# Performance work log

Hardware: AMD Instinct MI355X
Metric: run time of the kernel (lower is better)

Reference implementation:

```python
import jax, jax.numpy as jnp
import numpy as np

N = 100000
E = 1600000
D_IN = 128
D_OUT = 128
BN_EPS = 1e-5


def setup_inputs() -> dict:
    key = jax.random.key(0)
    k = jax.random.split(key, 8)
    feats = jax.random.normal(k[0], (N, D_IN), dtype=jnp.float32)
    src = jax.random.randint(k[1], (E,), 0, N, dtype=jnp.int32)
    dst = jax.random.randint(k[2], (E,), 0, N, dtype=jnp.int32)
    # GraphConv weight (in, out) + bias, residual Linear, batchnorm affine
    W = jax.random.normal(k[3], (D_IN, D_OUT), dtype=jnp.float32) / np.sqrt(D_IN)
    b = jnp.zeros((D_OUT,), dtype=jnp.float32)
    Wr = jax.random.normal(k[4], (D_IN, D_OUT), dtype=jnp.float32) / np.sqrt(D_IN)
    br = jnp.zeros((D_OUT,), dtype=jnp.float32)
    gamma = jnp.ones((D_OUT,), dtype=jnp.float32)
    beta = jnp.zeros((D_OUT,), dtype=jnp.float32)
    return {"feats": feats, "src": src, "dst": dst, "W": W, "b": b,
            "Wr": Wr, "br": br, "gamma": gamma, "beta": beta}


def reference(feats, src, dst, W, b, Wr, br, gamma, beta):
    ones = jnp.ones((src.shape[0],), dtype=feats.dtype)
    out_deg = jax.ops.segment_sum(ones, src, num_segments=N)
    in_deg = jax.ops.segment_sum(ones, dst, num_segments=N)
    norm_src = jax.lax.rsqrt(jnp.maximum(out_deg, 1.0))  # [N]
    norm_dst = jax.lax.rsqrt(jnp.maximum(in_deg, 1.0))   # [N]

    # GraphConv, norm='both' (in_feats == out_feats -> aggregate then matmul)
    h = feats * norm_src[:, None]
    agg = jax.ops.segment_sum(h[src], dst, num_segments=N)  # [N, D_IN]
    agg = agg * norm_dst[:, None]
    conv = jax.nn.relu(agg @ W + b)

    # residual linear + activation
    res = jax.nn.relu(feats @ Wr + br)
    y = conv + res  # dropout p=0 -> identity

    # BatchNorm1d (batch statistics, biased variance)
    mean = jnp.mean(y, axis=0)
    var = jnp.var(y, axis=0)
    y = (y - mean) * jax.lax.rsqrt(var + BN_EPS) * gamma + beta
    return y
```

## Files before the change

### kernel.cpp

```cpp
#include <hip/hip_runtime.h>

#define NN 100000
#define DD 128
#define EE 1600000
#define BN_EPS 1e-5f
#define NBLK 3125
#define NCH 2
#define CH 50000
#define CW (CH / 4)
#define NEB 64
#define EPB (EE / NEB)

using bf16x8 = __attribute__((ext_vector_type(8))) short;
using f32x4  = __attribute__((ext_vector_type(4))) float;

__device__ __forceinline__ unsigned short bf16r(float f) {
    unsigned u = __float_as_uint(f);
    u += 0x7FFF + ((u >> 16) & 1);
    return (unsigned short)(u >> 16);
}
__device__ __forceinline__ float bf2f(unsigned short h) {
    return __uint_as_float((unsigned)h << 16);
}

__global__ __launch_bounds__(1024) void hist_kernel(
    const int4* __restrict__ src4, const int4* __restrict__ dst4,
    unsigned char* __restrict__ outT8, unsigned char* __restrict__ inT8,
    unsigned char* __restrict__ lrank) {
    __shared__ unsigned outc[CW];
    __shared__ unsigned inc[CW];
    const int j = blockIdx.x & (NEB - 1);
    const int c = blockIdx.x >> 6;
    const int clo = c * CH;
    const int t = threadIdx.x;
    for (int i = t; i < CW; i += 1024) { outc[i] = 0; inc[i] = 0; }
    __syncthreads();
    const int base = j * (EPB / 4);
    for (int i = t; i < EPB / 4; i += 1024) {
        int4 s = src4[base + i];
        int4 d = dst4[base + i];
        int e = j * EPB + i * 4;
        unsigned sx = (unsigned)(s.x - clo);
        unsigned sy = (unsigned)(s.y - clo);
        unsigned sz = (unsigned)(s.z - clo);
        unsigned sw = (unsigned)(s.w - clo);
        if (sx < CH) atomicAdd(&outc[sx >> 2], 1u << ((sx & 3) * 8));
        if (sy < CH) atomicAdd(&outc[sy >> 2], 1u << ((sy & 3) * 8));
        if (sz < CH) atomicAdd(&outc[sz >> 2], 1u << ((sz & 3) * 8));
        if (sw < CH) atomicAdd(&outc[sw >> 2], 1u << ((sw & 3) * 8));
        unsigned dx = (unsigned)(d.x - clo);
        unsigned dy = (unsigned)(d.y - clo);
        unsigned dz = (unsigned)(d.z - clo);
        unsigned dw = (unsigned)(d.w - clo);
        if (dx < CH) { unsigned o = atomicAdd(&inc[dx >> 2], 1u << ((dx & 3) * 8)); lrank[e + 0] = (unsigned char)(o >> ((dx & 3) * 8)); }
        if (dy < CH) { unsigned o = atomicAdd(&inc[dy >> 2], 1u << ((dy & 3) * 8)); lrank[e + 1] = (unsigned char)(o >> ((dy & 3) * 8)); }
        if (dz < CH) { unsigned o = atomicAdd(&inc[dz >> 2], 1u << ((dz & 3) * 8)); lrank[e + 2] = (unsigned char)(o >> ((dz & 3) * 8)); }
        if (dw < CH) { unsigned o = atomicAdd(&inc[dw >> 2], 1u << ((dw & 3) * 8)); lrank[e + 3] = (unsigned char)(o >> ((dw & 3) * 8)); }
    }
    __syncthreads();
    unsigned* op = (unsigned*)(outT8 + (size_t)j * NN + clo);
    unsigned* ip = (unsigned*)(inT8 + (size_t)j * NN + clo);
    for (int i = t; i < CW; i += 1024) {
        op[i] = outc[i];
        ip[i] = inc[i];
    }
}

__global__ __launch_bounds__(1024) void scan1_kernel(
    const unsigned char* __restrict__ outT8, unsigned char* __restrict__ inT8,
    int* __restrict__ partial, int* __restrict__ blocksum,
    float* __restrict__ ns, float* __restrict__ nd) {
    __shared__ int s[1024];
    int t = threadIdx.x;
    int idx = blockIdx.x * 1024 + t;
    int run_in = 0;
    if (idx < NN) {
        int run_out = 0;
#pragma unroll 8
        for (int j = 0; j < NEB; ++j) {
            run_out += (int)outT8[(size_t)j * NN + idx];
            int ci = (int)inT8[(size_t)j * NN + idx];
            inT8[(size_t)j * NN + idx] = (unsigned char)run_in;
            run_in += ci;
        }
        ns[idx] = rsqrtf(fmaxf((float)run_out, 1.0f));
        nd[idx] = rsqrtf(fmaxf((float)run_in, 1.0f));
    }
    int v = run_in;
    s[t] = v;
    __syncthreads();
    for (int off = 1; off < 1024; off <<= 1) {
        int x = (t >= off) ? s[t - off] : 0;
        __syncthreads();
        s[t] += x;
        __syncthreads();
    }
    if (idx < NN) partial[idx] = s[t] - v;
    if (t == 1023) blocksum[blockIdx.x] = s[t];
}

__global__ void scan23_kernel(const int* __restrict__ partial, const int* __restrict__ blocksum,
                              int* __restrict__ row_ofs) {
    __shared__ int s[128];
    int t = threadIdx.x;
    if (t < 128) s[t] = (t < 98) ? blocksum[t] : 0;
    __syncthreads();
    for (int off = 1; off < 128; off <<= 1) {
        int x = (t < 128 && t >= off) ? s[t - off] : 0;
        __syncthreads();
        if (t < 128) s[t] += x;
        __syncthreads();
    }
    int i = blockIdx.x * blockDim.x + t;
    if (i < NN) {
        int bk = i >> 10;
        row_ofs[i] = partial[i] + s[bk] - blocksum[bk];
        if (i == 0) row_ofs[NN] = EE;
    }
}

__global__ void fill4_kernel(const int4* __restrict__ src4, const int4* __restrict__ dst4,
                             const unsigned char* __restrict__ baseT8,
                             const uchar4* __restrict__ lrank4,
                             const int* __restrict__ row_ofs, int* __restrict__ e_src) {
    int i = blockIdx.x * blockDim.x + threadIdx.x;
    if (i < EE / 4) {
        int4 s = src4[i];
        int4 d = dst4[i];
        uchar4 r = lrank4[i];
        int j = (i * 4) / EPB;
        const unsigned char* bT = baseT8 + (size_t)j * NN;
        e_src[row_ofs[d.x] + (int)bT[d.x] + (int)r.x] = s.x;
        e_src[row_ofs[d.y] + (int)bT[d.y] + (int)r.y] = s.y;
        e_src[row_ofs[d.z] + (int)bT[d.z] + (int)r.z] = s.z;
        e_src[row_ofs[d.w] + (int)bT[d.w] + (int)r.w] = s.w;
    }
}

__global__ void cvt_kernel(const float4* __restrict__ feats4, const float* __restrict__ ns,
                           ushort4* __restrict__ fb4) {
    int i = blockIdx.x * blockDim.x + threadIdx.x;
    if (i < NN * 32) {
        float s = ns[i >> 5];
        float4 v = feats4[i];
        ushort4 h;
        h.x = bf16r(v.x * s);
        h.y = bf16r(v.y * s);
        h.z = bf16r(v.z * s);
        h.w = bf16r(v.w * s);
        fb4[i] = h;
    }
}

__global__ void prepw_kernel(const float* __restrict__ W, const float* __restrict__ Wr,
                             unsigned short* __restrict__ wb) {
    int g = blockIdx.x >> 5;
    int f = blockIdx.x & 31;
    int ct = f >> 2, ks = f & 3;
    int l = threadIdx.x;
    const float* G = g ? Wr : W;
    unsigned short* hi = wb + (((size_t)(g * 2 + 0) * 32 + f) * 64 + l) * 8;
    unsigned short* lo = wb + (((size_t)(g * 2 + 1) * 32 + f) * 64 + l) * 8;
    for (int i = 0; i < 8; ++i) {
        int k = ks * 32 + (l >> 4) * 8 + i;
        int col = ct * 16 + (l & 15);
        float w = G[k * 128 + col];
        unsigned uh = __float_as_uint(w) & 0xFFFF0000u;
        hi[i] = (unsigned short)(uh >> 16);
        lo[i] = bf16r(w - __uint_as_float(uh));
    }
}

__device__ __forceinline__ void accum8(float* a, int4 u) {
    a[0] += __uint_as_float((unsigned)u.x << 16);
    a[1] += __uint_as_float((unsigned)u.x & 0xFFFF0000u);
    a[2] += __uint_as_float((unsigned)u.y << 16);
    a[3] += __uint_as_float((unsigned)u.y & 0xFFFF0000u);
    a[4] += __uint_as_float((unsigned)u.z << 16);
    a[5] += __uint_as_float((unsigned)u.z & 0xFFFF0000u);
    a[6] += __uint_as_float((unsigned)u.w << 16);
    a[7] += __uint_as_float((unsigned)u.w & 0xFFFF0000u);
}

__global__ __launch_bounds__(256, 6) void gather_kernel(
    const int4* __restrict__ fbi, const float* __restrict__ nd,
    const int* __restrict__ row_ofs, const int* __restrict__ e_src,
    float* __restrict__ y) {
    const int lane = threadIdx.x & 15;
    const int grp = threadIdx.x >> 4;
    const int node = blockIdx.x * 16 + grp;
    const int beg = row_ofs[node];
    const int end = row_ofs[node + 1];

    float a0[8] = {0.f, 0.f, 0.f, 0.f, 0.f, 0.f, 0.f, 0.f};
    float a1[8] = {0.f, 0.f, 0.f, 0.f, 0.f, 0.f, 0.f, 0.f};

    for (int e = beg; e < end; e += 16) {
        int cnt = end - e;
        if (cnt > 16) cnt = 16;
        int myidx = (lane < cnt) ? e_src[e + lane] : 0;
        int j = 0;
        for (; j + 7 < cnt; j += 8) {
            int s0 = __shfl(myidx, j, 16);
            int s1 = __shfl(myidx, j + 1, 16);
            int s2 = __shfl(myidx, j + 2, 16);
            int s3 = __shfl(myidx, j + 3, 16);
            int s4 = __shfl(myidx, j + 4, 16);
            int s5 = __shfl(myidx, j + 5, 16);
            int s6 = __shfl(myidx, j + 6, 16);
            int s7 = __shfl(myidx, j + 7, 16);
            int4 u0 = fbi[(size_t)s0 * 16 + lane];
            int4 u1 = fbi[(size_t)s1 * 16 + lane];
            int4 u2 = fbi[(size_t)s2 * 16 + lane];
            int4 u3 = fbi[(size_t)s3 * 16 + lane];
            int4 u4 = fbi[(size_t)s4 * 16 + lane];
            int4 u5 = fbi[(size_t)s5 * 16 + lane];
            int4 u6 = fbi[(size_t)s6 * 16 + lane];
            int4 u7 = fbi[(size_t)s7 * 16 + lane];
            accum8(a0, u0);
            accum8(a1, u1);
            accum8(a0, u2);
            accum8(a1, u3);
            accum8(a0, u4);
            accum8(a1, u5);
            accum8(a0, u6);
            accum8(a1, u7);
        }
        for (; j + 3 < cnt; j += 4) {
            int s0 = __shfl(myidx, j, 16);
            int s1 = __shfl(myidx, j + 1, 16);
            int s2 = __shfl(myidx, j + 2, 16);
            int s3 = __shfl(myidx, j + 3, 16);
            int4 u0 = fbi[(size_t)s0 * 16 + lane];
            int4 u1 = fbi[(size_t)s1 * 16 + lane];
            int4 u2 = fbi[(size_t)s2 * 16 + lane];
            int4 u3 = fbi[(size_t)s3 * 16 + lane];
            accum8(a0, u0);
            accum8(a1, u1);
            accum8(a0, u2);
            accum8(a1, u3);
        }
        for (; j < cnt; ++j) {
            int s0 = __shfl(myidx, j, 16);
            int4 u0 = fbi[(size_t)s0 * 16 + lane];
            accum8(a0, u0);
        }
    }

    float snd = nd[node];
    float4 o0, o1;
    o0.x = (a0[0] + a1[0]) * snd;
    o0.y = (a0[1] + a1[1]) * snd;
    o0.z = (a0[2] + a1[2]) * snd;
    o0.w = (a0[3] + a1[3]) * snd;
    o1.x = (a0[4] + a1[4]) * snd;
    o1.y = (a0[5] + a1[5]) * snd;
    o1.z = (a0[6] + a1[6]) * snd;
    o1.w = (a0[7] + a1[7]) * snd;
    ((float4*)y)[(size_t)node * 32 + lane * 2] = o0;
    ((float4*)y)[(size_t)node * 32 + lane * 2 + 1] = o1;
}

__device__ __forceinline__ void hilo4(float4 v, ushort4& h, ushort4& l) {
    unsigned u0 = __float_as_uint(v.x) & 0xFFFF0000u;
    unsigned u1 = __float_as_uint(v.y) & 0xFFFF0000u;
    unsigned u2 = __float_as_uint(v.z) & 0xFFFF0000u;
    unsigned u3 = __float_as_uint(v.w) & 0xFFFF0000u;
    h.x = (unsigned short)(u0 >> 16);
    h.y = (unsigned short)(u1 >> 16);
    h.z = (unsigned short)(u2 >> 16);
    h.w = (unsigned short)(u3 >> 16);
    l.x = bf16r(v.x - __uint_as_float(u0));
    l.y = bf16r(v.y - __uint_as_float(u1));
    l.z = bf16r(v.z - __uint_as_float(u2));
    l.w = bf16r(v.w - __uint_as_float(u3));
}

__global__ __launch_bounds__(256, 4) void gemm_kernel(
    const float4* __restrict__ feats4,
    const unsigned short* __restrict__ wb,
    const float* __restrict__ b, const float* __restrict__ br,
    float* y, float* __restrict__ part_sum, float* __restrict__ part_sq) {
    __shared__ unsigned short AsH[32 * 128];
    __shared__ unsigned short AsL[32 * 128];
    __shared__ unsigned short FsH[32 * 128];
    __shared__ unsigned short FsL[32 * 128];

    const int tid = threadIdx.x;
    const int block_row = blockIdx.x * 32;
    const float4* agg4 = (const float4*)y;

    for (int i = tid; i < 1024; i += 256) {
        int r = i >> 5;
        int c4 = i & 31;
        size_t g = (size_t)(block_row + r) * 32 + c4;
        float4 a = agg4[g];
        float4 f = feats4[g];
        int off = (r * 256 + ((c4 * 8) ^ ((r & 7) << 4))) >> 1;
        ushort4 h, l;
        hilo4(a, h, l);
        *(ushort4*)(&AsH[off]) = h;
        *(ushort4*)(&AsL[off]) = l;
        hilo4(f, h, l);
        *(ushort4*)(&FsH[off]) = h;
        *(ushort4*)(&FsL[off]) = l;
    }
    __syncthreads();

    const int w = tid >> 6;
    const int l = tid & 63;
    const int lr = l & 15;
    const int lh = l >> 4;
    const int ct0 = w * 2;
    const bf16x8* WB = (const bf16x8*)wb;

    const f32x4 fzero = {0.f, 0.f, 0.f, 0.f};
    f32x4 aC[2][2], aR[2][2];
#pragma unroll
    for (int r = 0; r < 2; ++r)
#pragma unroll
        for (int c = 0; c < 2; ++c) { aC[r][c] = fzero; aR[r][c] = fzero; }

#pragma unroll 1
    for (int ks = 0; ks < 4; ++ks) {
        bf16x8 ah[2], al[2], fh[2], fl[2];
#pragma unroll
        for (int r = 0; r < 2; ++r) {
            int row = r * 16 + lr;
            int off = (row * 256 + ((ks * 64 + lh * 16) ^ ((row & 7) << 4))) >> 1;
            ah[r] = *(const bf16x8*)(&AsH[off]);
            al[r] = *(const bf16x8*)(&AsL[off]);
            fh[r] = *(const bf16x8*)(&FsH[off]);
            fl[r] = *(const bf16x8*)(&FsL[off]);
        }
#pragma unroll
        for (int c = 0; c < 2; ++c) {
            int fr = (ct0 + c) * 4 + ks;
            bf16x8 wh  = WB[(0 * 32 + fr) * 64 + l];
            bf16x8 wl  = WB[(1 * 32 + fr) * 64 + l];
            bf16x8 wrh = WB[(2 * 32 + fr) * 64 + l];
            bf16x8 wrl = WB[(3 * 32 + fr) * 64 + l];
#pragma unroll
            for (int r = 0; r < 2; ++r) {
                aC[r][c] = __builtin_amdgcn_mfma_f32_16x16x32_bf16(ah[r], wh, aC[r][c], 0, 0, 0);
                aC[r][c] = __builtin_amdgcn_mfma_f32_16x16x32_bf16(al[r], wh, aC[r][c], 0, 0, 0);
                aC[r][c] = __builtin_amdgcn_mfma_f32_16x16x32_bf16(ah[r], wl, aC[r][c], 0, 0, 0);
                aR[r][c] = __builtin_amdgcn_mfma_f32_16x16x32_bf16(fh[r], wrh, aR[r][c], 0, 0, 0);
                aR[r][c] = __builtin_amdgcn_mfma_f32_16x16x32_bf16(fl[r], wrh, aR[r][c], 0, 0, 0);
                aR[r][c] = __builtin_amdgcn_mfma_f32_16x16x32_bf16(fh[r], wrl, aR[r][c], 0, 0, 0);
            }
        }
    }

#pragma unroll
    for (int c = 0; c < 2; ++c) {
        int col = (ct0 + c) * 16 + lr;
        float bv = b[col], brv = br[col];
        float cs = 0.f, cq = 0.f;
#pragma unroll
        for (int r = 0; r < 2; ++r) {
#pragma unroll
            for (int i = 0; i < 4; ++i) {
                float o = fmaxf(aC[r][c][i] + bv, 0.f) + fmaxf(aR[r][c][i] + brv, 0.f);
                int grow = block_row + r * 16 + lh * 4 + i;
                y[(size_t)grow * 128 + col] = o;
                cs += o;
                cq += o * o;
            }
        }
        cs += __shfl_xor(cs, 16); cs += __shfl_xor(cs, 32);
        cq += __shfl_xor(cq, 16); cq += __shfl_xor(cq, 32);
        if (lh == 0) {
            part_sum[(size_t)blockIdx.x * 128 + col] = cs;
            part_sq[(size_t)blockIdx.x * 128 + col] = cq;
        }
    }
}

__global__ __launch_bounds__(256) void colreduce_kernel(
    const float* __restrict__ part_sum, const float* __restrict__ part_sq,
    float* __restrict__ colsum, float* __restrict__ colsumsq) {
    int j = blockIdx.x;
    int t = threadIdx.x;
    float s = 0.f, q = 0.f;
    for (int bb = t; bb < NBLK; bb += 256) {
        s += part_sum[(size_t)bb * 128 + j];
        q += part_sq[(size_t)bb * 128 + j];
    }
#pragma unroll
    for (int off = 1; off < 64; off <<= 1) {
        s += __shfl_xor(s, off);
        q += __shfl_xor(q, off);
    }
    __shared__ float ss[4], qq[4];
    if ((t & 63) == 0) { ss[t >> 6] = s; qq[t >> 6] = q; }
    __syncthreads();
    if (t == 0) {
        colsum[j] = ss[0] + ss[1] + ss[2] + ss[3];
        colsumsq[j] = qq[0] + qq[1] + qq[2] + qq[3];
    }
}

__global__ void apply2_kernel(float4* __restrict__ y4,
                              const float* __restrict__ colsum, const float* __restrict__ colsumsq,
                              const float* __restrict__ gamma, const float* __restrict__ beta) {
    __shared__ float sc4[128], sh4[128];
    int t = threadIdx.x;
    if (t < 128) {
        const float inv_n = 1.0f / (float)NN;
        float mean = colsum[t] * inv_n;
        float var = colsumsq[t] * inv_n - mean * mean;
        float s = gamma[t] * rsqrtf(var + BN_EPS);
        sc4[t] = s;
        sh4[t] = beta[t] - mean * s;
    }
    __syncthreads();
    int i = blockIdx.x * 256 + t;
    if (i < NN * 32) {
        int c = (i & 31) * 4;
        float4 v = y4[i];
        v.x = v.x * sc4[c + 0] + sh4[c + 0];
        v.y = v.y * sc4[c + 1] + sh4[c + 1];
        v.z = v.z * sc4[c + 2] + sh4[c + 2];
        v.w = v.w * sc4[c + 3] + sh4[c + 3];
        y4[i] = v;
    }
}

extern "C" void kernel_launch(void* const* d_in, const int* in_sizes, int n_in,
                              void* d_out, int out_size, void* d_ws, size_t ws_size,
                              hipStream_t stream) {
    const float* feats = (const float*)d_in[0];
    const int* src = (const int*)d_in[1];
    const int* dst = (const int*)d_in[2];
    const float* W = (const float*)d_in[3];
    const float* b = (const float*)d_in[4];
    const float* Wr = (const float*)d_in[5];
    const float* br = (const float*)d_in[6];
    const float* gamma = (const float*)d_in[7];
    const float* beta = (const float*)d_in[8];
    float* y = (float*)d_out;

    char* ws = (char*)d_ws;
    unsigned char* outT8 = (unsigned char*)ws;
    unsigned char* inT8 = outT8 + (size_t)NEB * NN;
    unsigned char* lrank = inT8 + (size_t)NEB * NN;
    ushort4* fb4 = (ushort4*)ws;
    float* part_sum = (float*)lrank;
    float* part_sq = part_sum + (size_t)NBLK * 128;
    char* wsB = ws + (size_t)NN * 32 * 8;
    float* ns = (float*)wsB;
    float* nd = ns + NN;
    int* row_ofs = (int*)(nd + NN);
    int* partial = row_ofs + NN + 1;
    int* blocksum = partial + NN;
    int* e_src = blocksum + 128;
    float* colsum = (float*)(e_src + EE);
    float* colsumsq = colsum + DD;
    unsigned long long wbofs = (unsigned long long)((char*)(colsumsq + DD) - ws);
    wbofs = (wbofs + 255ull) & ~255ull;
    unsigned short* wb = (unsigned short*)(ws + wbofs);

    prepw_kernel<<<64, 64, 0, stream>>>(W, Wr, wb);
    hist_kernel<<<NCH * NEB, 1024, 0, stream>>>((const int4*)src, (const int4*)dst,
                                                outT8, inT8, lrank);
    scan1_kernel<<<98, 1024, 0, stream>>>(outT8, inT8, partial, blocksum, ns, nd);
    scan23_kernel<<<(NN + 255) / 256, 256, 0, stream>>>(partial, blocksum, row_ofs);
    fill4_kernel<<<(EE / 4 + 255) / 256, 256, 0, stream>>>((const int4*)src, (const int4*)dst,
                                                           inT8, (const uchar4*)lrank,
                                                           row_ofs, e_src);
    cvt_kernel<<<(NN * 32 + 255) / 256, 256, 0, stream>>>((const float4*)feats, ns, fb4);
    gather_kernel<<<NN / 16, 256, 0, stream>>>((const int4*)fb4, nd, row_ofs, e_src, y);
    gemm_kernel<<<NBLK, 256, 0, stream>>>((const float4*)feats, wb, b, br,
                                          y, part_sum, part_sq);
    colreduce_kernel<<<128, 256, 0, stream>>>(part_sum, part_sq, colsum, colsumsq);
    apply2_kernel<<<(NN * 32 + 255) / 256, 256, 0, stream>>>((float4*)y, colsum, colsumsq,
                                                             gamma, beta);
}
```

Measured before the change: 308.6 us.

## Fuse weight prep into hist kernel, chunk fill with LDS offsets, trim gather unroll

Weight splitting into bf16 hi/lo now runs as an extra block of the histogram kernel, which removes one launch. The edge fill kernel is restructured so each block handles one edge segment and a 25000-node destination chunk, with row offsets and base counts staged in shared memory. This replaces the scattered global lookups with LDS reads, but every block now rereads its edge segment four times. The 8-way unrolled loop in the gather kernel is removed, leaving the 4-way loop, which cuts register pressure at the cost of fewer loads in flight.

```diff
diff --git a/kernel.cpp b/kernel.cpp
--- a/kernel.cpp
+++ b/kernel.cpp
@@ -10,6 +10,7 @@
 #define CW (CH / 4)
 #define NEB 64
 #define EPB (EE / NEB)
+#define FCH 25000
 
 using bf16x8 = __attribute__((ext_vector_type(8))) short;
 using f32x4  = __attribute__((ext_vector_type(4))) float;
@@ -26,13 +27,37 @@
 __global__ __launch_bounds__(1024) void hist_kernel(
     const int4* __restrict__ src4, const int4* __restrict__ dst4,
     unsigned char* __restrict__ outT8, unsigned char* __restrict__ inT8,
-    unsigned char* __restrict__ lrank) {
+    unsigned char* __restrict__ lrank,
+    const float* __restrict__ W, const float* __restrict__ Wr,
+    unsigned short* __restrict__ wb) {
     __shared__ unsigned outc[CW];
     __shared__ unsigned inc[CW];
+    const int t = threadIdx.x;
+
+    if (blockIdx.x == NCH * NEB) {
+        for (int v = t; v < 4096; v += 1024) {
+            int bb = v >> 6, l = v & 63;
+            int g = bb >> 5, f = bb & 31;
+            int ks = f & 3;
+            int ct = f >> 2;
+            const float* G = g ? Wr : W;
+            unsigned short* hi = wb + (((size_t)(g * 2 + 0) * 32 + f) * 64 + l) * 8;
+            unsigned short* lo = wb + (((size_t)(g * 2 + 1) * 32 + f) * 64 + l) * 8;
+            for (int i = 0; i < 8; ++i) {
+                int k = ks * 32 + (l >> 4) * 8 + i;
+                int col = ct * 16 + (l & 15);
+                float w = G[k * 128 + col];
+                unsigned uh = __float_as_uint(w) & 0xFFFF0000u;
+                hi[i] = (unsigned short)(uh >> 16);
+                lo[i] = bf16r(w - __uint_as_float(uh));
+            }
+        }
+        return;
+    }
+
     const int j = blockIdx.x & (NEB - 1);
     const int c = blockIdx.x >> 6;
     const int clo = c * CH;
-    const int t = threadIdx.x;
     for (int i = t; i < CW; i += 1024) { outc[i] = 0; inc[i] = 0; }
     __syncthreads();
     const int base = j * (EPB / 4);
@@ -119,21 +144,36 @@
     }
 }
 
-__global__ void fill4_kernel(const int4* __restrict__ src4, const int4* __restrict__ dst4,
-                             const unsigned char* __restrict__ baseT8,
-                             const uchar4* __restrict__ lrank4,
-                             const int* __restrict__ row_ofs, int* __restrict__ e_src) {
-    int i = blockIdx.x * blockDim.x + threadIdx.x;
-    if (i < EE / 4) {
-        int4 s = src4[i];
-        int4 d = dst4[i];
-        uchar4 r = lrank4[i];
-        int j = (i * 4) / EPB;
-        const unsigned char* bT = baseT8 + (size_t)j * NN;
-        e_src[row_ofs[d.x] + (int)bT[d.x] + (int)r.x] = s.x;
-        e_src[row_ofs[d.y] + (int)bT[d.y] + (int)r.y] = s.y;
-        e_src[row_ofs[d.z] + (int)bT[d.z] + (int)r.z] = s.z;
-        e_src[row_ofs[d.w] + (int)bT[d.w] + (int)r.w] = s.w;
+__global__ __launch_bounds__(1024) void fill_kernel(
+    const int4* __restrict__ src4, const int4* __restrict__ dst4,
+    const unsigned char* __restrict__ baseT8, const uchar4* __restrict__ lrank4,
+    const int* __restrict__ row_ofs, int* __restrict__ e_src) {
+    __shared__ int ro_s[FCH];
+    __shared__ unsigned char ba_s[FCH];
+    const int j = blockIdx.x & (NEB - 1);
+    const int c = blockIdx.x >> 6;
+    const int clo = c * FCH;
+    const int t = threadIdx.x;
+    const unsigned char* bT = baseT8 + (size_t)j * NN + clo;
+    const int* roT = row_ofs + clo;
+    for (int i = t; i < FCH; i += 1024) {
+        ro_s[i] = roT[i];
+        ba_s[i] = bT[i];
+    }
+    __syncthreads();
+    const int base = j * (EPB / 4);
+    for (int i = t; i < EPB / 4; i += 1024) {
+        int4 s = src4[base + i];
+        int4 d = dst4[base + i];
+        uchar4 r = lrank4[base + i];
+        unsigned dx = (unsigned)(d.x - clo);
+        unsigned dy = (unsigned)(d.y - clo);
+        unsigned dz = (unsigned)(d.z - clo);
+        unsigned dw = (unsigned)(d.w - clo);
+        if (dx < FCH) e_src[ro_s[dx] + (int)ba_s[dx] + (int)r.x] = s.x;
+        if (dy < FCH) e_src[ro_s[dy] + (int)ba_s[dy] + (int)r.y] = s.y;
+        if (dz < FCH) e_src[ro_s[dz] + (int)ba_s[dz] + (int)r.z] = s.z;
+        if (dw < FCH) e_src[ro_s[dw] + (int)ba_s[dw] + (int)r.w] = s.w;
     }
 }
 
@@ -152,25 +192,6 @@
     }
 }
 
-__global__ void prepw_kernel(const float* __restrict__ W, const float* __restrict__ Wr,
-                             unsigned short* __restrict__ wb) {
-    int g = blockIdx.x >> 5;
-    int f = blockIdx.x & 31;
-    int ct = f >> 2, ks = f & 3;
-    int l = threadIdx.x;
-    const float* G = g ? Wr : W;
-    unsigned short* hi = wb + (((size_t)(g * 2 + 0) * 32 + f) * 64 + l) * 8;
-    unsigned short* lo = wb + (((size_t)(g * 2 + 1) * 32 + f) * 64 + l) * 8;
-    for (int i = 0; i < 8; ++i) {
-        int k = ks * 32 + (l >> 4) * 8 + i;
-        int col = ct * 16 + (l & 15);
-        float w = G[k * 128 + col];
-        unsigned uh = __float_as_uint(w) & 0xFFFF0000u;
-        hi[i] = (unsigned short)(uh >> 16);
-        lo[i] = bf16r(w - __uint_as_float(uh));
-    }
-}
-
 __device__ __forceinline__ void accum8(float* a, int4 u) {
     a[0] += __uint_as_float((unsigned)u.x << 16);
     a[1] += __uint_as_float((unsigned)u.x & 0xFFFF0000u);
@@ -200,32 +221,6 @@
         if (cnt > 16) cnt = 16;
         int myidx = (lane < cnt) ? e_src[e + lane] : 0;
         int j = 0;
-        for (; j + 7 < cnt; j += 8) {
-            int s0 = __shfl(myidx, j, 16);
-            int s1 = __shfl(myidx, j + 1, 16);
-            int s2 = __shfl(myidx, j + 2, 16);
-            int s3 = __shfl(myidx, j + 3, 16);
-            int s4 = __shfl(myidx, j + 4, 16);
-            int s5 = __shfl(myidx, j + 5, 16);
-            int s6 = __shfl(myidx, j + 6, 16);
-            int s7 = __shfl(myidx, j + 7, 16);
-            int4 u0 = fbi[(size_t)s0 * 16 + lane];
-            int4 u1 = fbi[(size_t)s1 * 16 + lane];
-            int4 u2 = fbi[(size_t)s2 * 16 + lane];
-            int4 u3 = fbi[(size_t)s3 * 16 + lane];
-            int4 u4 = fbi[(size_t)s4 * 16 + lane];
-            int4 u5 = fbi[(size_t)s5 * 16 + lane];
-            int4 u6 = fbi[(size_t)s6 * 16 + lane];
-            int4 u7 = fbi[(size_t)s7 * 16 + lane];
-            accum8(a0, u0);
-            accum8(a1, u1);
-            accum8(a0, u2);
-            accum8(a1, u3);
-            accum8(a0, u4);
-            accum8(a1, u5);
-            accum8(a0, u6);
-            accum8(a1, u7);
-        }
         for (; j + 3 < cnt; j += 4) {
             int s0 = __shfl(myidx, j, 16);
             int s1 = __shfl(myidx, j + 1, 16);
@@ -461,14 +456,12 @@
     wbofs = (wbofs + 255ull) & ~255ull;
     unsigned short* wb = (unsigned short*)(ws + wbofs);
 
-    prepw_kernel<<<64, 64, 0, stream>>>(W, Wr, wb);
-    hist_kernel<<<NCH * NEB, 1024, 0, stream>>>((const int4*)src, (const int4*)dst,
-                                                outT8, inT8, lrank);
+    hist_kernel<<<NCH * NEB + 1, 1024, 0, stream>>>((const int4*)src, (const int4*)dst,
+                                                    outT8, inT8, lrank, W, Wr, wb);
     scan1_kernel<<<98, 1024, 0, stream>>>(outT8, inT8, partial, blocksum, ns, nd);
     scan23_kernel<<<(NN + 255) / 256, 256, 0, stream>>>(partial, blocksum, row_ofs);
-    fill4_kernel<<<(EE / 4 + 255) / 256, 256, 0, stream>>>((const int4*)src, (const int4*)dst,
-                                                           inT8, (const uchar4*)lrank,
-                                                           row_ofs, e_src);
+    fill_kernel<<<4 * NEB, 1024, 0, stream>>>((const int4*)src, (const int4*)dst,
+                                              inT8, (const uchar4*)lrank, row_ofs, e_src);
     cvt_kernel<<<(NN * 32 + 255) / 256, 256, 0, stream>>>((const float4*)feats, ns, fb4);
     gather_kernel<<<NN / 16, 256, 0, stream>>>((const int4*)fb4, nd, row_ofs, e_src, y);
     gemm_kernel<<<NBLK, 256, 0, stream>>>((const float4*)feats, wb, b, br,
```

Result: faster. 297.6 us (-3.6%).
